# Performance work log

Hardware: AMD Instinct MI355X
Metric: run time of the kernel (lower is better)

The kernel has to match this reference:

```python
import jax, jax.numpy as jnp
import numpy as np

N_NODES = 100000
N_EDGES = 50000
NNZ = 1600000
IN_DIM, HID_DIM, N_CLASSES = 128, 128, 16


def setup_inputs() -> dict:
    key = jax.random.key(0)
    k1, k2, k3, k4, k5 = jax.random.split(key, 5)
    x = jax.random.normal(k1, (N_NODES, IN_DIM), dtype=jnp.float32)
    node_idx = jax.random.randint(k2, (NNZ,), 0, N_NODES, dtype=jnp.int64)
    edge_idx = jax.random.randint(k3, (NNZ,), 0, N_EDGES, dtype=jnp.int64)
    # glorot-ish weights, zero bias (PyG HypergraphConv: Linear(bias=False) + bias Parameter)
    W1 = jax.random.normal(k4, (IN_DIM, HID_DIM), dtype=jnp.float32) * (1.0 / np.sqrt(IN_DIM))
    b1 = jnp.zeros((HID_DIM,), dtype=jnp.float32)
    W2 = jax.random.normal(k5, (HID_DIM, N_CLASSES), dtype=jnp.float32) * (1.0 / np.sqrt(HID_DIM))
    b2 = jnp.zeros((N_CLASSES,), dtype=jnp.float32)
    return {"x": x, "node_idx": node_idx, "edge_idx": edge_idx, "num_edges": N_EDGES,
            "W1": W1, "b1": b1, "W2": W2, "b2": b2}


def hypergraph_conv(x, W, b, node_idx, edge_idx, num_edges):
    """PyG HypergraphConv (no attention, unit hyperedge weights):
       out = D^{-1} H B^{-1} H^T (x W) + b
    implemented as gather -> segment_sum (node->edge) -> gather -> segment_sum (edge->node)."""
    n_nodes = x.shape[0]
    ones = jnp.ones(node_idx.shape[0], dtype=x.dtype)
    deg = jax.ops.segment_sum(ones, node_idx, num_segments=n_nodes)      # D: node degree
    edeg = jax.ops.segment_sum(ones, edge_idx, num_segments=num_edges)   # B: hyperedge size
    Dinv = jnp.where(deg > 0, 1.0 / deg, 0.0)
    Binv = jnp.where(edeg > 0, 1.0 / edeg, 0.0)

    xw = x @ W                                                            # [N, F_out]
    # node -> hyperedge, norm = B^{-1} applied per message (indexed by edge)
    msg_ne = xw[node_idx] * Binv[edge_idx][:, None]                       # [nnz, F_out]
    e_feat = jax.ops.segment_sum(msg_ne, edge_idx, num_segments=num_edges)
    # hyperedge -> node, norm = D^{-1} applied per message (indexed by node)
    msg_en = e_feat[edge_idx] * Dinv[node_idx][:, None]                   # [nnz, F_out]
    out = jax.ops.segment_sum(msg_en, node_idx, num_segments=n_nodes)
    return out + b


def reference(x, node_idx, edge_idx, num_edges, W1, b1, W2, b2):
    # Dropout is inactive in eval mode; model is relu(conv1) -> conv2.
    h = jax.nn.relu(hypergraph_conv(x, W1, b1, node_idx, edge_idx, num_edges))
    return hypergraph_conv(h, W2, b2, node_idx, edge_idx, num_edges)
```

## Files before the change

kernel.cpp:

```cpp
#include <hip/hip_runtime.h>
#include <hip/hip_fp16.h>


#define N_EDGES_C 50000
#define F1 128
#define F2 16
#define CHUNK 4096
#define EBIN_SHIFT 7
#define NBIN_SHIFT 8
#define EBINS 391
#define NBINS 391

typedef __attribute__((ext_vector_type(8))) _Float16 half8;
typedef __attribute__((ext_vector_type(4))) float f32x4;


__global__ __launch_bounds__(256) void hist_chunk_kernel(
    const int* __restrict__ node_idx, const int* __restrict__ edge_idx,
    int* __restrict__ echunkcnt, int* __restrict__ nchunkcnt, int nnz) {
  __shared__ int ebc[EBINS], nbc[NBINS];
  const int t = threadIdx.x;
  for (int b = t; b < EBINS; b += 256) ebc[b] = 0;
  for (int b = t; b < NBINS; b += 256) nbc[b] = 0;
  __syncthreads();
  const int base = blockIdx.x * CHUNK;
  int end = base + CHUNK; if (end > nnz) end = nnz;
  for (int i = base + t; i < end; i += 256) {
    atomicAdd(&ebc[edge_idx[i] >> EBIN_SHIFT], 1);
    atomicAdd(&nbc[node_idx[i] >> NBIN_SHIFT], 1);
  }
  __syncthreads();
  const int nC = gridDim.x;
  for (int b = t; b < EBINS; b += 256) echunkcnt[b * nC + blockIdx.x] = ebc[b];
  for (int b = t; b < NBINS; b += 256) nchunkcnt[b * nC + blockIdx.x] = nbc[b];
}

__global__ __launch_bounds__(256) void cscan_p1_kernel(
    const int* __restrict__ ecc, const int* __restrict__ ncc,
    int* __restrict__ epart, int* __restrict__ npart,
    int Le, int Ln, int nbE) {
  __shared__ int red[256];
  const int t = threadIdx.x;
  const int b = blockIdx.x;
  const int* src; int L; int* dst; int bb;
  if (b < nbE) { src = ecc; L = Le; dst = epart; bb = b; }
  else         { src = ncc; L = Ln; dst = npart; bb = b - nbE; }
  int base = bb * 1024 + t * 4;
  int s = 0;
#pragma unroll
  for (int j = 0; j < 4; ++j) { int i = base + j; if (i < L) s += src[i]; }
  red[t] = s;
  __syncthreads();
  for (int d = 128; d > 0; d >>= 1) {
    if (t < d) red[t] += red[t + d];
    __syncthreads();
  }
  if (t == 0) dst[bb] = red[0];
}

__global__ __launch_bounds__(256) void cscan_p2_kernel(
    int* __restrict__ epart, int* __restrict__ npart,
    int* __restrict__ ebinbase, int* __restrict__ nbinbase,
    int nbE, int nbN, int nnz) {
  __shared__ int se[256], sn[256];
  const int t = threadIdx.x;
  se[t] = (t < nbE) ? epart[t] : 0;
  sn[t] = (t < nbN) ? npart[t] : 0;
  __syncthreads();
  for (int d = 1; d < 256; d <<= 1) {
    int ve = (t >= d) ? se[t - d] : 0;
    int vn = (t >= d) ? sn[t - d] : 0;
    __syncthreads();
    se[t] += ve; sn[t] += vn;
    __syncthreads();
  }
  if (t < nbE) epart[t] = (t > 0) ? se[t - 1] : 0;
  if (t < nbN) npart[t] = (t > 0) ? sn[t - 1] : 0;
  if (t == 0) { ebinbase[EBINS] = nnz; nbinbase[NBINS] = nnz; }
}

__global__ __launch_bounds__(256) void cscan_p3_kernel(
    const int* __restrict__ ecc, const int* __restrict__ ncc,
    const int* __restrict__ epart, const int* __restrict__ npart,
    int* __restrict__ erunoff, int* __restrict__ nrunoff,
    int* __restrict__ ebinbase, int* __restrict__ nbinbase,
    int Le, int Ln, int nbE, int nC) {
  __shared__ int red[256];
  const int t = threadIdx.x;
  const int b = blockIdx.x;
  const int* src; const int* part; int L; int* ro; int* bba; int bb;
  if (b < nbE) { src = ecc; part = epart; L = Le; ro = erunoff; bba = ebinbase; bb = b; }
  else         { src = ncc; part = npart; L = Ln; ro = nrunoff; bba = nbinbase; bb = b - nbE; }
  int base = bb * 1024 + t * 4;
  int v[4]; int s = 0;
#pragma unroll
  for (int j = 0; j < 4; ++j) { int i = base + j; v[j] = (i < L) ? src[i] : 0; s += v[j]; }
  red[t] = s;
  __syncthreads();
  for (int d = 1; d < 256; d <<= 1) {
    int x = (t >= d) ? red[t - d] : 0;
    __syncthreads();
    red[t] += x;
    __syncthreads();
  }
  int run = part[bb] + ((t > 0) ? red[t - 1] : 0);
#pragma unroll
  for (int j = 0; j < 4; ++j) {
    int i = base + j;
    if (i < L) {
      ro[i] = run;
      if (i % nC == 0) bba[i / nC] = run;
      run += v[j];
    }
  }
}

__global__ __launch_bounds__(256) void stage_kernel(
    const int* __restrict__ node_idx, const int* __restrict__ edge_idx,
    const int* __restrict__ erunoff, const int* __restrict__ nrunoff,
    int2* __restrict__ epairs, int2* __restrict__ npairs, int nnz) {
  __shared__ int ecur[EBINS], ncur[NBINS];
  const int t = threadIdx.x;
  const int nC = gridDim.x;
  for (int b = t; b < EBINS; b += 256) ecur[b] = erunoff[b * nC + blockIdx.x];
  for (int b = t; b < NBINS; b += 256) ncur[b] = nrunoff[b * nC + blockIdx.x];
  __syncthreads();
  const int base = blockIdx.x * CHUNK;
  int end = base + CHUNK; if (end > nnz) end = nnz;
  for (int i = base + t; i < end; i += 256) {
    int e = edge_idx[i];
    int n = node_idx[i];
    int p = atomicAdd(&ecur[e >> EBIN_SHIFT], 1);
    epairs[p] = make_int2(e, n);
    int q = atomicAdd(&ncur[n >> NBIN_SHIFT], 1);
    npairs[q] = make_int2(n, e);
  }
}

__global__ __launch_bounds__(256) void bin_scatter_kernel(
    const int2* __restrict__ epairs, const int2* __restrict__ npairs,
    const int* __restrict__ ebinbase, const int* __restrict__ nbinbase,
    int* __restrict__ eoff, int* __restrict__ noff,
    int* __restrict__ enbr, int* __restrict__ nnbr,
    int n_edges, int n_nodes) {
  __shared__ int cnt[256];
  __shared__ int scn[256];
  const int bid = blockIdx.x;
  const int t = threadIdx.x;
  if (bid < EBINS) {
    const int e0 = bid << EBIN_SHIFT;
    const int ne = min(1 << EBIN_SHIFT, n_edges - e0);
    const int beg = ebinbase[bid], end = ebinbase[bid + 1];
    if (t < 128) cnt[t] = 0;
    __syncthreads();
    for (int j = beg + t; j < end; j += 256) atomicAdd(&cnt[epairs[j].x & 127], 1);
    __syncthreads();
    if (t < 128) scn[t] = cnt[t];
    __syncthreads();
    for (int d = 1; d < 128; d <<= 1) {
      int x = 0;
      if (t < 128 && t >= d) x = scn[t - d];
      __syncthreads();
      if (t < 128) scn[t] += x;
      __syncthreads();
    }
    int pos0 = 0;
    if (t < 128) {
      int excl = (t > 0) ? scn[t - 1] : 0;
      pos0 = beg + excl;
      if (t < ne) eoff[e0 + t] = pos0;
    }
    __syncthreads();
    if (t < 128) scn[t] = pos0;
    __syncthreads();
    for (int j = beg + t; j < end; j += 256) {
      int2 p = epairs[j];
      int pos = atomicAdd(&scn[p.x & 127], 1);
      enbr[pos] = p.y;
    }
    if (bid == EBINS - 1 && t == 0) eoff[n_edges] = end;
  } else {
    const int b = bid - EBINS;
    const int n0 = b << NBIN_SHIFT;
    const int nn = min(1 << NBIN_SHIFT, n_nodes - n0);
    const int beg = nbinbase[b], end = nbinbase[b + 1];
    cnt[t] = 0;
    __syncthreads();
    for (int j = beg + t; j < end; j += 256) atomicAdd(&cnt[npairs[j].x & 255], 1);
    __syncthreads();
    scn[t] = cnt[t];
    __syncthreads();
    for (int d = 1; d < 256; d <<= 1) {
      int x = (t >= d) ? scn[t - d] : 0;
      __syncthreads();
      scn[t] += x;
      __syncthreads();
    }
    int excl = (t > 0) ? scn[t - 1] : 0;
    int pos0 = beg + excl;
    if (t < nn) noff[n0 + t] = pos0;
    __syncthreads();
    scn[t] = pos0;
    __syncthreads();
    for (int j = beg + t; j < end; j += 256) {
      int2 p = npairs[j];
      int pos = atomicAdd(&scn[p.x & 255], 1);
      nnbr[pos] = p.y;
    }
    if (bid == EBINS + NBINS - 1 && t == 0) noff[n_nodes] = end;
  }
}


__global__ __launch_bounds__(256) void w1t_kernel(
    const float* __restrict__ W1, __half* __restrict__ W1t) {
  int i = blockIdx.x * 256 + threadIdx.x;
  int n = i >> 7, k = i & 127;
  W1t[i] = __float2half(W1[k * 128 + n]);
}


__global__ __launch_bounds__(256) void gemm1_kernel(
    const float* __restrict__ A, const __half* __restrict__ W1t16,
    __half* __restrict__ C16, int M) {
  __shared__ _Float16 As[64 * 136];
  __shared__ _Float16 Bs[128 * 136];
  const int t = threadIdx.x;
  const int bm = blockIdx.x * 64;

#pragma unroll
  for (int i = 0; i < 8; ++i) {
    int lin = i * 256 + t;
    int row = lin >> 5;
    int c4 = lin & 31;
    int grow = bm + row;
    float4 v = make_float4(0.f, 0.f, 0.f, 0.f);
    if (grow < M) v = *(const float4*)(A + (size_t)grow * 128 + c4 * 4);
    _Float16* dst = &As[row * 136 + c4 * 4];
    dst[0] = (_Float16)v.x; dst[1] = (_Float16)v.y;
    dst[2] = (_Float16)v.z; dst[3] = (_Float16)v.w;
  }
#pragma unroll
  for (int i = 0; i < 8; ++i) {
    int lin = i * 256 + t;
    int n = lin >> 4;
    int c = lin & 15;
    *(float4*)&Bs[n * 136 + c * 8] = *(const float4*)(W1t16 + n * 128 + c * 8);
  }
  __syncthreads();

  const int w = t >> 6;
  const int lane = t & 63;
  const int l16 = lane & 15;
  const int quad = lane >> 4;

  f32x4 acc[8];
#pragma unroll
  for (int n = 0; n < 8; ++n) acc[n] = (f32x4){0.f, 0.f, 0.f, 0.f};

  const _Float16* arow = &As[(w * 16 + l16) * 136 + quad * 8];
#pragma unroll
  for (int kt = 0; kt < 4; ++kt) {
    half8 a = *(const half8*)(arow + kt * 32);
#pragma unroll
    for (int n = 0; n < 8; ++n) {
      half8 b = *(const half8*)&Bs[(n * 16 + l16) * 136 + kt * 32 + quad * 8];
      acc[n] = __builtin_amdgcn_mfma_f32_16x16x32_f16(a, b, acc[n], 0, 0, 0);
    }
  }
  __syncthreads();

#pragma unroll
  for (int n = 0; n < 8; ++n) {
#pragma unroll
    for (int r = 0; r < 4; ++r) {
      int row = w * 16 + quad * 4 + r;
      int col = n * 16 + l16;
      As[row * 136 + col] = (_Float16)acc[n][r];
    }
  }
  __syncthreads();

#pragma unroll
  for (int i = 0; i < 4; ++i) {
    int lin = i * 256 + t;
    int row = lin >> 4;
    int c = lin & 15;
    int grow = bm + row;
    if (grow < M)
      *(float4*)(C16 + (size_t)grow * 128 + c * 8) = *(const float4*)&As[row * 136 + c * 8];
  }
}


__device__ __forceinline__ void acc_h8(float* ax, float4 v) {
  const __half2* h = (const __half2*)&v;
#pragma unroll
  for (int q = 0; q < 4; ++q) {
    float2 f = __half22float2(h[q]);
    ax[2 * q] += f.x; ax[2 * q + 1] += f.y;
  }
}

__global__ __launch_bounds__(256) void edge_agg128_kernel(
    const float4* __restrict__ feat,
    const int* __restrict__ nbr, const int* __restrict__ off,
    float4* __restrict__ outf, int nseg) {
  int w = (blockIdx.x * 256 + threadIdx.x) >> 6;
  if (w >= nseg) return;
  const int lane = threadIdx.x & 63;
  const int r = lane >> 4;
  const int f = lane & 15;
  int beg = off[w], end = off[w + 1];
  float ax[8];
#pragma unroll
  for (int i = 0; i < 8; ++i) ax[i] = 0.f;
  int k = beg + r;
  for (; k + 12 < end; k += 16) {
    int n0 = nbr[k], n1 = nbr[k + 4], n2 = nbr[k + 8], n3 = nbr[k + 12];
    float4 v0 = feat[(size_t)n0 * 16 + f];
    float4 v1 = feat[(size_t)n1 * 16 + f];
    float4 v2 = feat[(size_t)n2 * 16 + f];
    float4 v3 = feat[(size_t)n3 * 16 + f];
    acc_h8(ax, v0); acc_h8(ax, v1); acc_h8(ax, v2); acc_h8(ax, v3);
  }
  for (; k < end; k += 4) acc_h8(ax, feat[(size_t)nbr[k] * 16 + f]);
#pragma unroll
  for (int i = 0; i < 8; ++i) {
    ax[i] += __shfl_xor(ax[i], 16, 64);
    ax[i] += __shfl_xor(ax[i], 32, 64);
  }
  if (r == 0) {
    float inv = (end > beg) ? 1.f / (float)(end - beg) : 0.f;
    union { float4 f4; __half2 h[4]; } u;
#pragma unroll
    for (int q = 0; q < 4; ++q)
      u.h[q] = __floats2half2_rn(ax[2 * q] * inv, ax[2 * q + 1] * inv);
    outf[(size_t)w * 16 + f] = u.f4;
  }
}

__global__ __launch_bounds__(256) void node_agg128_kernel(
    const float4* __restrict__ feat,
    const int* __restrict__ nbr, const int* __restrict__ off,
    const float* __restrict__ bias,
    float4* __restrict__ outf, int nseg) {
  int w = (blockIdx.x * 256 + threadIdx.x) >> 6;
  if (w >= nseg) return;
  const int lane = threadIdx.x & 63;
  const int r = lane >> 4;
  const int f = lane & 15;
  int beg = off[w], end = off[w + 1];
  float ax[8];
#pragma unroll
  for (int i = 0; i < 8; ++i) ax[i] = 0.f;
  int k = beg + r;
  for (; k + 12 < end; k += 16) {
    int e0 = nbr[k], e1 = nbr[k + 4], e2 = nbr[k + 8], e3 = nbr[k + 12];
    float4 v0 = feat[(size_t)e0 * 16 + f];
    float4 v1 = feat[(size_t)e1 * 16 + f];
    float4 v2 = feat[(size_t)e2 * 16 + f];
    float4 v3 = feat[(size_t)e3 * 16 + f];
    acc_h8(ax, v0); acc_h8(ax, v1); acc_h8(ax, v2); acc_h8(ax, v3);
  }
  for (; k < end; k += 4) acc_h8(ax, feat[(size_t)nbr[k] * 16 + f]);
#pragma unroll
  for (int i = 0; i < 8; ++i) {
    ax[i] += __shfl_xor(ax[i], 16, 64);
    ax[i] += __shfl_xor(ax[i], 32, 64);
  }
  if (r == 0) {
    float inv = (end > beg) ? 1.f / (float)(end - beg) : 0.f;
    float4 blo = ((const float4*)bias)[2 * f];
    float4 bhi = ((const float4*)bias)[2 * f + 1];
    float bb[8] = {blo.x, blo.y, blo.z, blo.w, bhi.x, bhi.y, bhi.z, bhi.w};
    union { float4 f4; __half2 h[4]; } u;
#pragma unroll
    for (int q = 0; q < 4; ++q) {
      float hx = fmaxf(ax[2 * q] * inv + bb[2 * q], 0.f);
      float hy = fmaxf(ax[2 * q + 1] * inv + bb[2 * q + 1], 0.f);
      u.h[q] = __floats2half2_rn(hx, hy);
    }
    outf[(size_t)w * 16 + f] = u.f4;
  }
}


__global__ __launch_bounds__(256) void gemm2_kernel(
    const __half* __restrict__ H16, const float* __restrict__ W2,
    __half2* __restrict__ O16, int M) {
  __shared__ float ws2[128 * 16];
  const int t = threadIdx.x;
#pragma unroll
  for (int i = 0; i < 8; ++i) ws2[i * 256 + t] = W2[i * 256 + t];
  __syncthreads();

  int r0 = blockIdx.x * 512 + t;
  int r1 = r0 + 256;
  bool v0 = r0 < M, v1 = r1 < M;
  const __half2* h0 = (const __half2*)(H16 + (size_t)r0 * 128);
  const __half2* h1 = (const __half2*)(H16 + (size_t)r1 * 128);

  float4 acc0[4], acc1[4];
#pragma unroll
  for (int q = 0; q < 4; ++q) {
    acc0[q] = make_float4(0.f, 0.f, 0.f, 0.f);
    acc1[q] = make_float4(0.f, 0.f, 0.f, 0.f);
  }

  for (int k4 = 0; k4 < 32; ++k4) {
    float2 f00 = make_float2(0.f, 0.f), f01 = make_float2(0.f, 0.f);
    float2 f10 = make_float2(0.f, 0.f), f11 = make_float2(0.f, 0.f);
    if (v0) { f00 = __half22float2(h0[2 * k4]); f01 = __half22float2(h0[2 * k4 + 1]); }
    if (v1) { f10 = __half22float2(h1[2 * k4]); f11 = __half22float2(h1[2 * k4 + 1]); }
    const float a0s[4] = {f00.x, f00.y, f01.x, f01.y};
    const float a1s[4] = {f10.x, f10.y, f11.x, f11.y};
#pragma unroll
    for (int j = 0; j < 4; ++j) {
      int k = k4 * 4 + j;
#pragma unroll
      for (int q = 0; q < 4; ++q) {
        float4 b = *(const float4*)&ws2[k * 16 + q * 4];
        acc0[q].x = fmaf(a0s[j], b.x, acc0[q].x);
        acc0[q].y = fmaf(a0s[j], b.y, acc0[q].y);
        acc0[q].z = fmaf(a0s[j], b.z, acc0[q].z);
        acc0[q].w = fmaf(a0s[j], b.w, acc0[q].w);
        acc1[q].x = fmaf(a1s[j], b.x, acc1[q].x);
        acc1[q].y = fmaf(a1s[j], b.y, acc1[q].y);
        acc1[q].z = fmaf(a1s[j], b.z, acc1[q].z);
        acc1[q].w = fmaf(a1s[j], b.w, acc1[q].w);
      }
    }
  }
  if (v0) {
    __half2* op = O16 + (size_t)r0 * 8;
#pragma unroll
    for (int q = 0; q < 4; ++q) {
      op[q * 2]     = __floats2half2_rn(acc0[q].x, acc0[q].y);
      op[q * 2 + 1] = __floats2half2_rn(acc0[q].z, acc0[q].w);
    }
  }
  if (v1) {
    __half2* op = O16 + (size_t)r1 * 8;
#pragma unroll
    for (int q = 0; q < 4; ++q) {
      op[q * 2]     = __floats2half2_rn(acc1[q].x, acc1[q].y);
      op[q * 2 + 1] = __floats2half2_rn(acc1[q].z, acc1[q].w);
    }
  }
}


__global__ __launch_bounds__(256) void edge_agg16_kernel(
    const __half* __restrict__ feat, const int* __restrict__ nbr,
    const int* __restrict__ off, float* __restrict__ outf, int nseg) {
  int gid = blockIdx.x * 256 + threadIdx.x;
  int seg = gid >> 4;
  int c = gid & 15;
  if (seg >= nseg) return;
  int beg = off[seg], end = off[seg + 1];
  float a0 = 0.f, a1 = 0.f, a2 = 0.f, a3 = 0.f;
  int j = beg;
  for (; j + 8 <= end; j += 8) {
    int n0 = nbr[j],     n1 = nbr[j + 1], n2 = nbr[j + 2], n3 = nbr[j + 3];
    int n4 = nbr[j + 4], n5 = nbr[j + 5], n6 = nbr[j + 6], n7 = nbr[j + 7];
    float v0 = __half2float(feat[(size_t)n0 * 16 + c]);
    float v1 = __half2float(feat[(size_t)n1 * 16 + c]);
    float v2 = __half2float(feat[(size_t)n2 * 16 + c]);
    float v3 = __half2float(feat[(size_t)n3 * 16 + c]);
    float v4 = __half2float(feat[(size_t)n4 * 16 + c]);
    float v5 = __half2float(feat[(size_t)n5 * 16 + c]);
    float v6 = __half2float(feat[(size_t)n6 * 16 + c]);
    float v7 = __half2float(feat[(size_t)n7 * 16 + c]);
    a0 += v0 + v4; a1 += v1 + v5; a2 += v2 + v6; a3 += v3 + v7;
  }
  for (; j < end; ++j) a0 += __half2float(feat[(size_t)nbr[j] * 16 + c]);
  float inv = (end > beg) ? 1.f / (float)(end - beg) : 0.f;
  outf[(size_t)seg * 16 + c] = ((a0 + a1) + (a2 + a3)) * inv;
}

__global__ __launch_bounds__(256) void node_agg16_kernel(
    const float* __restrict__ feat, const int* __restrict__ nbr,
    const int* __restrict__ off, const float* __restrict__ bias,
    float* __restrict__ outf, int nseg) {
  int gid = blockIdx.x * 256 + threadIdx.x;
  int seg = gid >> 4;
  int c = gid & 15;
  if (seg >= nseg) return;
  int beg = off[seg], end = off[seg + 1];
  float a0 = 0.f, a1 = 0.f, a2 = 0.f, a3 = 0.f;
  int j = beg;
  for (; j + 8 <= end; j += 8) {
    int n0 = nbr[j],     n1 = nbr[j + 1], n2 = nbr[j + 2], n3 = nbr[j + 3];
    int n4 = nbr[j + 4], n5 = nbr[j + 5], n6 = nbr[j + 6], n7 = nbr[j + 7];
    float v0 = feat[(size_t)n0 * 16 + c];
    float v1 = feat[(size_t)n1 * 16 + c];
    float v2 = feat[(size_t)n2 * 16 + c];
    float v3 = feat[(size_t)n3 * 16 + c];
    float v4 = feat[(size_t)n4 * 16 + c];
    float v5 = feat[(size_t)n5 * 16 + c];
    float v6 = feat[(size_t)n6 * 16 + c];
    float v7 = feat[(size_t)n7 * 16 + c];
    a0 += v0 + v4; a1 += v1 + v5; a2 += v2 + v6; a3 += v3 + v7;
  }
  for (; j < end; ++j) a0 += feat[(size_t)nbr[j] * 16 + c];
  float inv = (end > beg) ? 1.f / (float)(end - beg) : 0.f;
  outf[(size_t)seg * 16 + c] = ((a0 + a1) + (a2 + a3)) * inv + bias[c];
}


extern "C" void kernel_launch(void* const* d_in, const int* in_sizes, int n_in,
                              void* d_out, int out_size, void* d_ws, size_t ws_size,
                              hipStream_t stream) {
  const float* x        = (const float*)d_in[0];
  const int*   node_idx = (const int*)d_in[1];
  const int*   edge_idx = (const int*)d_in[2];
  const float* W1 = (const float*)d_in[4];
  const float* b1 = (const float*)d_in[5];
  const float* W2 = (const float*)d_in[6];
  const float* b2 = (const float*)d_in[7];
  float* out = (float*)d_out;

  const int n_nodes = in_sizes[0] / F1;
  const int nnz     = in_sizes[1];
  const int n_edges = N_EDGES_C;
  const int nC      = (nnz + CHUNK - 1) / CHUNK;
  const int Le      = EBINS * nC;
  const int Ln      = NBINS * nC;
  const int nbE     = (Le + 1023) / 1024;
  const int nbN     = (Ln + 1023) / 1024;

  char* ws = (char*)d_ws;
  int2*    epairs = (int2*)(ws + 0);
  int2*    npairs = (int2*)(ws + 12800000);
  __half*  h16    = (__half*)(ws + 0);
  __half*  xw16   = (__half*)(ws + 25600000);
  __half*  ef16   = (__half*)(ws + 51200000);
  __half*  hw216  = (__half*)(ws + 64000000);
  float*   ef2    = (float*)(ws + 70400000);
  int*     enbr   = (int*)(ws + 73600000);
  int*     nnbr   = (int*)(ws + 80000000);
  int*     eoff   = (int*)(ws + 86400000);
  int*     noff   = (int*)(ws + 86600008);
  int*     echunkcnt = (int*)(ws + 87000016);
  int*     nchunkcnt = (int*)(ws + 87611540);
  int*     erunoff   = (int*)(ws + 88223064);
  int*     nrunoff   = (int*)(ws + 88834588);
  int*     ebinbase  = (int*)(ws + 89446112);
  int*     nbinbase  = (int*)(ws + 89447680);
  int*     epart     = (int*)(ws + 89449248);
  int*     npart     = (int*)(ws + 89450272);
  __half*  w1t16     = (__half*)(ws + 89451520);

  w1t_kernel<<<64, 256, 0, stream>>>(W1, w1t16);

  hist_chunk_kernel<<<nC, 256, 0, stream>>>(node_idx, edge_idx,
                                            echunkcnt, nchunkcnt, nnz);
  cscan_p1_kernel<<<nbE + nbN, 256, 0, stream>>>(echunkcnt, nchunkcnt,
                                                 epart, npart, Le, Ln, nbE);
  cscan_p2_kernel<<<1, 256, 0, stream>>>(epart, npart, ebinbase, nbinbase,
                                         nbE, nbN, nnz);
  cscan_p3_kernel<<<nbE + nbN, 256, 0, stream>>>(echunkcnt, nchunkcnt,
                                                 epart, npart, erunoff, nrunoff,
                                                 ebinbase, nbinbase, Le, Ln, nbE, nC);
  stage_kernel<<<nC, 256, 0, stream>>>(node_idx, edge_idx, erunoff, nrunoff,
                                       epairs, npairs, nnz);
  bin_scatter_kernel<<<EBINS + NBINS, 256, 0, stream>>>(epairs, npairs,
                                                        ebinbase, nbinbase,
                                                        eoff, noff, enbr, nnbr,
                                                        n_edges, n_nodes);

  gemm1_kernel<<<(n_nodes + 63) / 64, 256, 0, stream>>>(x, w1t16, xw16, n_nodes);
  edge_agg128_kernel<<<(n_edges * 64 + 255) / 256, 256, 0, stream>>>(
      (const float4*)xw16, enbr, eoff, (float4*)ef16, n_edges);
  node_agg128_kernel<<<(n_nodes * 64 + 255) / 256, 256, 0, stream>>>(
      (const float4*)ef16, nnbr, noff, b1, (float4*)h16, n_nodes);

  gemm2_kernel<<<(n_nodes + 511) / 512, 256, 0, stream>>>(h16, W2,
                                                          (__half2*)hw216, n_nodes);
  edge_agg16_kernel<<<(n_edges * 16 + 255) / 256, 256, 0, stream>>>(
      hw216, enbr, eoff, ef2, n_edges);
  node_agg16_kernel<<<(n_nodes * 16 + 255) / 256, 256, 0, stream>>>(
      ef2, nnbr, noff, b2, out, n_nodes);
}
```

Before: 374.3 us.

## Split 128-wide features into 16-wide slices and store node neighbor lists as ushort

gemm1 now writes its fp16 output in a slice-major layout of 8 slices, each [M][16]. The 128-feature aggregation kernels process one slice per group of warps, so each gather pass works on a smaller feature array that is more likely to stay in cache. Node-side neighbor indices are stored as 16-bit values, which is valid because there are fewer than 65536 edges, and index loads and output stores now use nontemporal hints. In exchange, each gather fetches only 32 bytes per row, and the neighbor index lists are re-read once per slice.

```diff
diff --git a/kernel.cpp b/kernel.cpp
--- a/kernel.cpp
+++ b/kernel.cpp
@@ -13,6 +13,7 @@
 
 typedef __attribute__((ext_vector_type(8))) _Float16 half8;
 typedef __attribute__((ext_vector_type(4))) float f32x4;
+typedef unsigned short ushort16_t;
 
 
 __global__ __launch_bounds__(256) void hist_chunk_kernel(
@@ -141,7 +142,7 @@
     const int2* __restrict__ epairs, const int2* __restrict__ npairs,
     const int* __restrict__ ebinbase, const int* __restrict__ nbinbase,
     int* __restrict__ eoff, int* __restrict__ noff,
-    int* __restrict__ enbr, int* __restrict__ nnbr,
+    int* __restrict__ enbr, ushort16_t* __restrict__ nnbr,
     int n_edges, int n_nodes) {
   __shared__ int cnt[256];
   __shared__ int scn[256];
@@ -205,7 +206,7 @@
     for (int j = beg + t; j < end; j += 256) {
       int2 p = npairs[j];
       int pos = atomicAdd(&scn[p.x & 255], 1);
-      nnbr[pos] = p.y;
+      nnbr[pos] = (ushort16_t)p.y;
     }
     if (bid == EBINS + NBINS - 1 && t == 0) noff[n_nodes] = end;
   }
@@ -284,16 +285,20 @@
 #pragma unroll
   for (int i = 0; i < 4; ++i) {
     int lin = i * 256 + t;
-    int row = lin >> 4;
-    int c = lin & 15;
+    int f = lin & 1;
+    int rlo = (lin >> 1) & 1;
+    int sl = (lin >> 2) & 7;
+    int rhi = lin >> 5;
+    int row = rhi * 2 + rlo;
     int grow = bm + row;
     if (grow < M)
-      *(float4*)(C16 + (size_t)grow * 128 + c * 8) = *(const float4*)&As[row * 136 + c * 8];
-  }
-}
-
-
-__device__ __forceinline__ void acc_h8(float* ax, float4 v) {
+      *(float4*)(C16 + ((size_t)sl * M + grow) * 16 + f * 8) =
+          *(const float4*)&As[row * 136 + sl * 16 + f * 8];
+  }
+}
+
+
+__device__ __forceinline__ void acc_h8(float* ax, f32x4 v) {
   const __half2* h = (const __half2*)&v;
 #pragma unroll
   for (int q = 0; q < 4; ++q) {
@@ -302,86 +307,109 @@
   }
 }
 
-__global__ __launch_bounds__(256) void edge_agg128_kernel(
-    const float4* __restrict__ feat,
-    const int* __restrict__ nbr, const int* __restrict__ off,
-    float4* __restrict__ outf, int nseg) {
-  int w = (blockIdx.x * 256 + threadIdx.x) >> 6;
-  if (w >= nseg) return;
+__global__ __launch_bounds__(256) void edge_agg128s_kernel(
+    const f32x4* __restrict__ feat,
+    const int* __restrict__ nbr,
+    const int* __restrict__ off,
+    f32x4* __restrict__ outf,
+    int nseg, int n_n, int wps) {
+  int gw = (blockIdx.x * 256 + threadIdx.x) >> 6;
+  int s = gw / wps;
+  int lw = gw - s * wps;
   const int lane = threadIdx.x & 63;
-  const int r = lane >> 4;
-  const int f = lane & 15;
-  int beg = off[w], end = off[w + 1];
+  int seg = lw * 4 + (lane >> 4);
+  const int r = (lane >> 1) & 7;
+  const int f = lane & 1;
+  int beg = 0, end = 0;
+  if (seg < nseg) { beg = off[seg]; end = off[seg + 1]; }
+  const f32x4* fs = feat + (size_t)s * n_n * 2;
   float ax[8];
 #pragma unroll
   for (int i = 0; i < 8; ++i) ax[i] = 0.f;
   int k = beg + r;
-  for (; k + 12 < end; k += 16) {
-    int n0 = nbr[k], n1 = nbr[k + 4], n2 = nbr[k + 8], n3 = nbr[k + 12];
-    float4 v0 = feat[(size_t)n0 * 16 + f];
-    float4 v1 = feat[(size_t)n1 * 16 + f];
-    float4 v2 = feat[(size_t)n2 * 16 + f];
-    float4 v3 = feat[(size_t)n3 * 16 + f];
+  for (; k + 24 < end; k += 32) {
+    int e0 = __builtin_nontemporal_load(&nbr[k]);
+    int e1 = __builtin_nontemporal_load(&nbr[k + 8]);
+    int e2 = __builtin_nontemporal_load(&nbr[k + 16]);
+    int e3 = __builtin_nontemporal_load(&nbr[k + 24]);
+    f32x4 v0 = fs[(size_t)e0 * 2 + f];
+    f32x4 v1 = fs[(size_t)e1 * 2 + f];
+    f32x4 v2 = fs[(size_t)e2 * 2 + f];
+    f32x4 v3 = fs[(size_t)e3 * 2 + f];
     acc_h8(ax, v0); acc_h8(ax, v1); acc_h8(ax, v2); acc_h8(ax, v3);
   }
-  for (; k < end; k += 4) acc_h8(ax, feat[(size_t)nbr[k] * 16 + f]);
+  for (; k < end; k += 8) {
+    int e0 = __builtin_nontemporal_load(&nbr[k]);
+    acc_h8(ax, fs[(size_t)e0 * 2 + f]);
+  }
 #pragma unroll
   for (int i = 0; i < 8; ++i) {
-    ax[i] += __shfl_xor(ax[i], 16, 64);
-    ax[i] += __shfl_xor(ax[i], 32, 64);
-  }
-  if (r == 0) {
+    ax[i] += __shfl_xor(ax[i], 2, 64);
+    ax[i] += __shfl_xor(ax[i], 4, 64);
+    ax[i] += __shfl_xor(ax[i], 8, 64);
+  }
+  if (r == 0 && seg < nseg) {
     float inv = (end > beg) ? 1.f / (float)(end - beg) : 0.f;
-    union { float4 f4; __half2 h[4]; } u;
+    union { f32x4 f4; __half2 h[4]; } u;
 #pragma unroll
     for (int q = 0; q < 4; ++q)
       u.h[q] = __floats2half2_rn(ax[2 * q] * inv, ax[2 * q + 1] * inv);
-    outf[(size_t)w * 16 + f] = u.f4;
-  }
-}
-
-__global__ __launch_bounds__(256) void node_agg128_kernel(
-    const float4* __restrict__ feat,
-    const int* __restrict__ nbr, const int* __restrict__ off,
+    __builtin_nontemporal_store(u.f4, &outf[((size_t)s * nseg + seg) * 2 + f]);
+  }
+}
+
+__global__ __launch_bounds__(256) void node_agg128s_kernel(
+    const f32x4* __restrict__ feat,
+    const ushort16_t* __restrict__ nbr,
+    const int* __restrict__ off,
     const float* __restrict__ bias,
-    float4* __restrict__ outf, int nseg) {
-  int w = (blockIdx.x * 256 + threadIdx.x) >> 6;
-  if (w >= nseg) return;
+    f32x4* __restrict__ outf,
+    int nseg, int n_e, int wps) {
+  int gw = (blockIdx.x * 256 + threadIdx.x) >> 6;
+  int s = gw / wps;
+  int lw = gw - s * wps;
   const int lane = threadIdx.x & 63;
-  const int r = lane >> 4;
-  const int f = lane & 15;
-  int beg = off[w], end = off[w + 1];
+  int seg = lw * 4 + (lane >> 4);
+  const int r = (lane >> 1) & 7;
+  const int f = lane & 1;
+  int beg = 0, end = 0;
+  if (seg < nseg) { beg = off[seg]; end = off[seg + 1]; }
+  const f32x4* fs = feat + (size_t)s * n_e * 2;
   float ax[8];
 #pragma unroll
   for (int i = 0; i < 8; ++i) ax[i] = 0.f;
   int k = beg + r;
-  for (; k + 12 < end; k += 16) {
-    int e0 = nbr[k], e1 = nbr[k + 4], e2 = nbr[k + 8], e3 = nbr[k + 12];
-    float4 v0 = feat[(size_t)e0 * 16 + f];
-    float4 v1 = feat[(size_t)e1 * 16 + f];
-    float4 v2 = feat[(size_t)e2 * 16 + f];
-    float4 v3 = feat[(size_t)e3 * 16 + f];
-    acc_h8(ax, v0); acc_h8(ax, v1); acc_h8(ax, v2); acc_h8(ax, v3);
-  }
-  for (; k < end; k += 4) acc_h8(ax, feat[(size_t)nbr[k] * 16 + f]);
+  for (; k + 8 < end; k += 16) {
+    int e0 = __builtin_nontemporal_load(&nbr[k]);
+    int e1 = __builtin_nontemporal_load(&nbr[k + 8]);
+    f32x4 v0 = fs[(size_t)e0 * 2 + f];
+    f32x4 v1 = fs[(size_t)e1 * 2 + f];
+    acc_h8(ax, v0); acc_h8(ax, v1);
+  }
+  for (; k < end; k += 8) {
+    int e0 = __builtin_nontemporal_load(&nbr[k]);
+    acc_h8(ax, fs[(size_t)e0 * 2 + f]);
+  }
 #pragma unroll
   for (int i = 0; i < 8; ++i) {
-    ax[i] += __shfl_xor(ax[i], 16, 64);
-    ax[i] += __shfl_xor(ax[i], 32, 64);
-  }
-  if (r == 0) {
+    ax[i] += __shfl_xor(ax[i], 2, 64);
+    ax[i] += __shfl_xor(ax[i], 4, 64);
+    ax[i] += __shfl_xor(ax[i], 8, 64);
+  }
+  if (r == 0 && seg < nseg) {
     float inv = (end > beg) ? 1.f / (float)(end - beg) : 0.f;
-    float4 blo = ((const float4*)bias)[2 * f];
-    float4 bhi = ((const float4*)bias)[2 * f + 1];
+    const float4* b4 = (const float4*)bias;
+    float4 blo = b4[s * 4 + f * 2];
+    float4 bhi = b4[s * 4 + f * 2 + 1];
     float bb[8] = {blo.x, blo.y, blo.z, blo.w, bhi.x, bhi.y, bhi.z, bhi.w};
-    union { float4 f4; __half2 h[4]; } u;
+    union { f32x4 f4; __half2 h[4]; } u;
 #pragma unroll
     for (int q = 0; q < 4; ++q) {
       float hx = fmaxf(ax[2 * q] * inv + bb[2 * q], 0.f);
       float hy = fmaxf(ax[2 * q + 1] * inv + bb[2 * q + 1], 0.f);
       u.h[q] = __floats2half2_rn(hx, hy);
     }
-    outf[(size_t)w * 16 + f] = u.f4;
+    __builtin_nontemporal_store(u.f4, &outf[((size_t)s * nseg + seg) * 2 + f]);
   }
 }
 
@@ -398,8 +426,6 @@
   int r0 = blockIdx.x * 512 + t;
   int r1 = r0 + 256;
   bool v0 = r0 < M, v1 = r1 < M;
-  const __half2* h0 = (const __half2*)(H16 + (size_t)r0 * 128);
-  const __half2* h1 = (const __half2*)(H16 + (size_t)r1 * 128);
 
   float4 acc0[4], acc1[4];
 #pragma unroll
@@ -408,27 +434,32 @@
     acc1[q] = make_float4(0.f, 0.f, 0.f, 0.f);
   }
 
-  for (int k4 = 0; k4 < 32; ++k4) {
-    float2 f00 = make_float2(0.f, 0.f), f01 = make_float2(0.f, 0.f);
-    float2 f10 = make_float2(0.f, 0.f), f11 = make_float2(0.f, 0.f);
-    if (v0) { f00 = __half22float2(h0[2 * k4]); f01 = __half22float2(h0[2 * k4 + 1]); }
-    if (v1) { f10 = __half22float2(h1[2 * k4]); f11 = __half22float2(h1[2 * k4 + 1]); }
-    const float a0s[4] = {f00.x, f00.y, f01.x, f01.y};
-    const float a1s[4] = {f10.x, f10.y, f11.x, f11.y};
-#pragma unroll
-    for (int j = 0; j < 4; ++j) {
-      int k = k4 * 4 + j;
-#pragma unroll
-      for (int q = 0; q < 4; ++q) {
-        float4 b = *(const float4*)&ws2[k * 16 + q * 4];
-        acc0[q].x = fmaf(a0s[j], b.x, acc0[q].x);
-        acc0[q].y = fmaf(a0s[j], b.y, acc0[q].y);
-        acc0[q].z = fmaf(a0s[j], b.z, acc0[q].z);
-        acc0[q].w = fmaf(a0s[j], b.w, acc0[q].w);
-        acc1[q].x = fmaf(a1s[j], b.x, acc1[q].x);
-        acc1[q].y = fmaf(a1s[j], b.y, acc1[q].y);
-        acc1[q].z = fmaf(a1s[j], b.z, acc1[q].z);
-        acc1[q].w = fmaf(a1s[j], b.w, acc1[q].w);
+  for (int sl = 0; sl < 8; ++sl) {
+    const __half2* h0 = (const __half2*)(H16 + ((size_t)sl * M + r0) * 16);
+    const __half2* h1 = (const __half2*)(H16 + ((size_t)sl * M + r1) * 16);
+#pragma unroll
+    for (int k4 = 0; k4 < 4; ++k4) {
+      float2 f00 = make_float2(0.f, 0.f), f01 = make_float2(0.f, 0.f);
+      float2 f10 = make_float2(0.f, 0.f), f11 = make_float2(0.f, 0.f);
+      if (v0) { f00 = __half22float2(h0[2 * k4]); f01 = __half22float2(h0[2 * k4 + 1]); }
+      if (v1) { f10 = __half22float2(h1[2 * k4]); f11 = __half22float2(h1[2 * k4 + 1]); }
+      const float a0s[4] = {f00.x, f00.y, f01.x, f01.y};
+      const float a1s[4] = {f10.x, f10.y, f11.x, f11.y};
+#pragma unroll
+      for (int j = 0; j < 4; ++j) {
+        int k = sl * 16 + k4 * 4 + j;
+#pragma unroll
+        for (int q = 0; q < 4; ++q) {
+          float4 b = *(const float4*)&ws2[k * 16 + q * 4];
+          acc0[q].x = fmaf(a0s[j], b.x, acc0[q].x);
+          acc0[q].y = fmaf(a0s[j], b.y, acc0[q].y);
+          acc0[q].z = fmaf(a0s[j], b.z, acc0[q].z);
+          acc0[q].w = fmaf(a0s[j], b.w, acc0[q].w);
+          acc1[q].x = fmaf(a1s[j], b.x, acc1[q].x);
+          acc1[q].y = fmaf(a1s[j], b.y, acc1[q].y);
+          acc1[q].z = fmaf(a1s[j], b.z, acc1[q].z);
+          acc1[q].w = fmaf(a1s[j], b.w, acc1[q].w);
+        }
       }
     }
   }
@@ -480,7 +511,7 @@
 }
 
 __global__ __launch_bounds__(256) void node_agg16_kernel(
-    const float* __restrict__ feat, const int* __restrict__ nbr,
+    const float* __restrict__ feat, const ushort16_t* __restrict__ nbr,
     const int* __restrict__ off, const float* __restrict__ bias,
     float* __restrict__ outf, int nseg) {
   int gid = blockIdx.x * 256 + threadIdx.x;
@@ -539,7 +570,7 @@
   __half*  hw216  = (__half*)(ws + 64000000);
   float*   ef2    = (float*)(ws + 70400000);
   int*     enbr   = (int*)(ws + 73600000);
-  int*     nnbr   = (int*)(ws + 80000000);
+  ushort16_t* nnbr16 = (ushort16_t*)(ws + 80000000);
   int*     eoff   = (int*)(ws + 86400000);
   int*     noff   = (int*)(ws + 86600008);
   int*     echunkcnt = (int*)(ws + 87000016);
@@ -567,19 +598,21 @@
                                        epairs, npairs, nnz);
   bin_scatter_kernel<<<EBINS + NBINS, 256, 0, stream>>>(epairs, npairs,
                                                         ebinbase, nbinbase,
-                                                        eoff, noff, enbr, nnbr,
+                                                        eoff, noff, enbr, nnbr16,
                                                         n_edges, n_nodes);
 
   gemm1_kernel<<<(n_nodes + 63) / 64, 256, 0, stream>>>(x, w1t16, xw16, n_nodes);
-  edge_agg128_kernel<<<(n_edges * 64 + 255) / 256, 256, 0, stream>>>(
-      (const float4*)xw16, enbr, eoff, (float4*)ef16, n_edges);
-  node_agg128_kernel<<<(n_nodes * 64 + 255) / 256, 256, 0, stream>>>(
-      (const float4*)ef16, nnbr, noff, b1, (float4*)h16, n_nodes);
+  const int wpsE = (n_edges + 3) / 4;
+  const int wpsN = (n_nodes + 3) / 4;
+  edge_agg128s_kernel<<<2 * wpsE, 256, 0, stream>>>(
+      (const f32x4*)xw16, enbr, eoff, (f32x4*)ef16, n_edges, n_nodes, wpsE);
+  node_agg128s_kernel<<<2 * wpsN, 256, 0, stream>>>(
+      (const f32x4*)ef16, nnbr16, noff, b1, (f32x4*)h16, n_nodes, n_edges, wpsN);
 
   gemm2_kernel<<<(n_nodes + 511) / 512, 256, 0, stream>>>(h16, W2,
                                                           (__half2*)hw216, n_nodes);
   edge_agg16_kernel<<<(n_edges * 16 + 255) / 256, 256, 0, stream>>>(
       hw216, enbr, eoff, ef2, n_edges);
   node_agg16_kernel<<<(n_nodes * 16 + 255) / 256, 256, 0, stream>>>(
-      ef2, nnbr, noff, b2, out, n_nodes);
-}
+      ef2, nnbr16, noff, b2, out, n_nodes);
+}
```

After: 471.7 us. 26.0% more time.
